# Optimization experiments

Hardware: AMD Instinct MI355X
Metric: run time of the kernel (lower is better)

Reference implementation:

```python
import jax, jax.numpy as jnp
import numpy as np

LATENT_SHAPES = [(192, 2, 2), (48, 4, 4), (24, 8, 8), (12, 16, 16), (6, 32, 32)]
B = 4          # batch
M = 32         # num_bases
HT, WT = 32, 32  # target spatial size = spatial size of z[-1] = (H/2, W/2)
EPS = 1e-3
CT = sum(s[0] for s in LATENT_SHAPES)  # 282


def _forward_fft(zs):
    # strided zero-insertion upsample of each latent to (HT, WT), concat channels, 2D FFT
    ups = []
    for zi in zs:
        b, c, h, w = zi.shape
        rh, rw = HT // h, WT // w
        u = jnp.zeros((b, c, HT, WT), zi.dtype).at[..., ::rh, ::rw].set(zi)
        ups.append(u)
    z = jnp.concatenate(ups, axis=1)            # (B, CT, HT, WT)
    return jnp.fft.fftn(z, axes=(-2, -1))       # complex64


def _inverse_fft(v_fft):
    # inverse FFT, take real part, split channels per level, strided downsample
    v = jnp.fft.ifftn(v_fft, axes=(-2, -1)).real  # (B, M, CT, HT, WT)
    splits = np.cumsum([s[0] for s in LATENT_SHAPES])[:-1]
    parts = jnp.split(v, splits, axis=-3)
    out = []
    for vi, (c, h, w) in zip(parts, LATENT_SHAPES):
        rh, rw = HT // h, WT // w
        out.append(vi[..., ::rh, ::rw])           # (B, M, c, h, w)
    return out


def _vector_field(zs, L, lam):
    z_fft = _forward_fft(zs)
    La = (L - jnp.swapaxes(L, -1, -2)).astype(jnp.complex64)        # antisymmetric (M, CT, CT)
    lam_a = (lam - jnp.roll(jnp.flip(lam, (1, 2)), (1, 1), axis=(1, 2))) * 1j  # (M, HT, WT) imaginary
    v_fft = jnp.einsum('mcd,bchw->bmdhw', La, z_fft)                 # (B, M, CT, HT, WT) complex
    v_fft = v_fft * lam_a[None, :, None, :, :]
    return _inverse_fft(v_fft)


def _log_prob(ws, zs, L, lam):
    S_ww = sum(jnp.einsum('bchw,bchw->b', wi, wi) for wi in ws)      # (B,)
    v = _vector_field(zs, L, lam)
    S_zz = sum(jnp.einsum('bnchw,bmchw->bnm', vi, vi) for vi in v)   # (B, M, M)
    S_zw = sum(jnp.einsum('bnchw,bchw->bn', vi, wi) for vi, wi in zip(v, ws))  # (B, M)
    var = jnp.maximum(jnp.mean(jnp.diagonal(S_zz, axis1=-2, axis2=-1), -1), 1e-6)
    std = jnp.sqrt(var)
    S_zz = S_zz / var[:, None, None]
    S_zw = S_zw / std[:, None]
    I = jnp.eye(M, dtype=S_zz.dtype)
    Mm = S_zz + EPS * I
    trace = EPS * S_ww + jnp.einsum('bn,bn->b', S_zw, S_zw)
    Lh = jnp.linalg.cholesky(Mm)
    logdet = 2.0 * jnp.sum(jnp.log(jnp.diagonal(Lh, axis1=-2, axis2=-1)), -1)
    return 0.5 * (logdet - trace)


def setup_inputs() -> dict:
    key = jax.random.key(0)
    ks = jax.random.split(key, 12)
    inp = {}
    for i, (c, h, w) in enumerate(LATENT_SHAPES):
        inp[f'z{i}'] = jax.random.normal(ks[i], (B, c, h, w), jnp.float32)
        inp[f'w{i}'] = jax.random.normal(ks[5 + i], (B, c, h, w), jnp.float32)
    inp['L'] = jax.random.normal(ks[10], (M, CT, CT), jnp.float32) * np.float32(1.0 / np.sqrt(CT))
    inp['lam'] = jax.random.normal(ks[11], (M, HT, WT), jnp.float32)
    return inp


def reference(z0, z1, z2, z3, z4, w0, w1, w2, w3, w4, L, lam):
    return _log_prob([w0, w1, w2, w3, w4], [z0, z1, z2, z3, z4], L, lam)
```

## Files before the change

### kernel.cpp

```cpp
#include <hip/hip_runtime.h>
#include <math.h>

#define NB 4
#define NM 32
#define CTOT 282
#define EPSV 1e-3f

__constant__ int g_cL[5]   = {192,48,24,12,6};
__constant__ int g_hL[5]   = {2,4,8,16,32};
__constant__ int g_coff[5] = {0,192,240,264,276};
__constant__ int g_zo[5]   = {0,768,1536,3072,6144};
__constant__ int g_po[4]   = {0,4,20,84};

__constant__ int t_lo[48] = {0,0,0,0,0,0,0,0,0,0,0,0,0,0,0,0,
                             0,0,0,0,0,0,0,0,0,0,0,0,0,0,0,0,
                             1,1,1,1,1,1,1,1, 2,2,2,2, 3,3, 4,4};
__constant__ int t_d0[48] = {0,6,12,18,24,30,36,42,48,54,60,66,72,78,84,90,
                             96,102,108,114,120,126,132,138,144,150,156,162,168,174,180,186,
                             192,198,204,210,216,222,228,234, 240,246,252,258, 264,270, 276,279};
__constant__ int t_nd[48] = {6,6,6,6,6,6,6,6,6,6,6,6,6,6,6,6,
                             6,6,6,6,6,6,6,6,6,6,6,6,6,6,6,6,
                             6,6,6,6,6,6,6,6, 6,6,6,6, 6,6, 3,3};

__constant__ int dft_l[30]  = {0,0,0, 1,1,1, 2,2,2,2,2,2,
                               3,3,3,3,3,3,3,3,3,3,3,3, 4,4,4,4,4,4};
__constant__ int dft_c0[30] = {0,64,128, 0,16,32, 0,4,8,12,16,20,
                               0,1,2,3,4,5,6,7,8,9,10,11, 0,1,2,3,4,5};
__constant__ int dft_nc[30] = {64,64,64, 16,16,16, 4,4,4,4,4,4,
                               1,1,1,1,1,1,1,1,1,1,1,1, 1,1,1,1,1,1};

#define N_LA     (NM*CTOT*CTOT)
#define OFF_LAT  0
#define OFF_ZRE  (OFF_LAT + N_LA)
#define OFF_ZIM  (OFF_ZRE + NB*12288)
#define OFF_WRE  (OFF_ZIM + NB*12288)
#define OFF_WIM  (OFF_WRE + NB*12288)
#define OFF_LAM  (OFF_WIM + NB*12288)
#define OFF_LAMF (OFF_LAM + NM*1024)
#define OFF_ZTR  (OFF_LAMF + NM*340)
#define OFF_ZTI  (OFF_ZTR + NB*6144)
#define OFF_UR   (OFF_ZTI + NB*6144)
#define OFF_UI   (OFF_UR + NB*NM*2720)
#define OFF_VRE  (OFF_UI + NB*NM*2720)
#define OFF_VIM  (OFF_VRE + NB*NM*12288)
#define OFF_SZZ  (OFF_VIM + NB*NM*12288)
#define OFF_SZW  (OFF_SZZ + NB*NM*NM)
#define OFF_SWW  (OFF_SZW + NB*NM)

#define PRE_LAT   (NM*25)
#define PRE_LAMF  (PRE_LAT + NM)
#define PRE_DFT   (PRE_LAMF + 2*NB*30)
#define PRE_SWW   (PRE_DFT + NB)
#define PRE_ZERO  (PRE_SWW + 17)

__global__ void __launch_bounds__(256) k_pre(
    const float* z0,const float* z1,const float* z2,const float* z3,const float* z4,
    const float* w0,const float* w1,const float* w2,const float* w3,const float* w4,
    const float* __restrict__ L, const float* __restrict__ lam, float* __restrict__ ws){
  __shared__ float shm[4160];
  int bid = blockIdx.x, t = threadIdx.x;
  if (bid < PRE_LAT){
    int m = bid/25, tl = bid%25;
    int d0 = (tl/5)*64, c0 = (tl%5)*64;
    const float* Lm = L + (size_t)m*CTOT*CTOT;
    float* At = shm;
    for (int i=t;i<4096;i+=256){
      int r=i>>6, c=i&63;
      At[r*65+c] = (c0+r<CTOT && d0+c<CTOT) ? Lm[(size_t)(c0+r)*CTOT + d0+c] : 0.f;
    }
    __syncthreads();
    float* out = ws + OFF_LAT + (size_t)m*CTOT*CTOT;
    for (int i=t;i<4096;i+=256){
      int r=i>>6, c=i&63;
      if (d0+r<CTOT && c0+c<CTOT)
        out[(size_t)(d0+r)*CTOT + c0+c] = At[c*65+r] - Lm[(size_t)(d0+r)*CTOT + c0+c];
    }
    return;
  }
  if (bid < PRE_LAMF){
    float* sA = shm;
    float* f3 = shm + 1024;
    float* f2 = shm + 1280;
    float* f1 = shm + 1344;
    int m = bid - PRE_LAT;
    for (int k=t;k<1024;k+=256){
      int ky=k>>5, kx=k&31;
      int nk = (((32-ky)&31)<<5) | ((32-kx)&31);
      float v = lam[(m<<10)+k] - lam[(m<<10)+nk];
      sA[k]=v;
      ws[OFF_LAM+(m<<10)+k]=v;
    }
    __syncthreads();
    { int s=t; int ky=s>>4, kx=s&15;
      float v = sA[(ky<<5)+kx]+sA[((ky+16)<<5)+kx]+sA[(ky<<5)+kx+16]+sA[((ky+16)<<5)+kx+16];
      f3[s]=v; ws[OFF_LAMF+m*340+84+s]=v; }
    __syncthreads();
    if (t<64){ int ky=t>>3, kx=t&7;
      float v = f3[(ky<<4)+kx]+f3[((ky+8)<<4)+kx]+f3[(ky<<4)+kx+8]+f3[((ky+8)<<4)+kx+8];
      f2[t]=v; ws[OFF_LAMF+m*340+20+t]=v; }
    __syncthreads();
    if (t<16){ int ky=t>>2, kx=t&3;
      float v = f2[(ky<<3)+kx]+f2[((ky+4)<<3)+kx]+f2[(ky<<3)+kx+4]+f2[((ky+4)<<3)+kx+4];
      f1[t]=v; ws[OFF_LAMF+m*340+4+t]=v; }
    __syncthreads();
    if (t<4){ int ky=t>>1, kx=t&1;
      float v = f1[(ky<<2)+kx]+f1[((ky+2)<<2)+kx]+f1[(ky<<2)+kx+2]+f1[((ky+2)<<2)+kx+2];
      ws[OFF_LAMF+m*340+t]=v; }
    return;
  }
  if (bid < PRE_DFT){
    float* sIn = shm;
    float* s1r = shm + 1024;
    float* s1i = shm + 2080;
    float* lc  = shm + 3136;
    float* lsn = shm + 3168;
    int i0 = bid - PRE_LAMF;
    int which = i0 / (NB*30);
    int rem = i0 % (NB*30);
    int b = rem / 30, j = rem % 30;
    int l = dft_l[j], c0 = dft_c0[j], nc = dft_nc[j];
    int h = g_hL[l], n = h*h;
    int hp = h+1, n1 = h*hp;
    int mult = 32/h;
    int elems = nc*n;
    const float* src;
    switch (which*5 + l){
      case 0: src=z0; break; case 1: src=z1; break; case 2: src=z2; break;
      case 3: src=z3; break; case 4: src=z4; break;
      case 5: src=w0; break; case 6: src=w1; break; case 7: src=w2; break;
      case 8: src=w3; break; default: src=w4; break;
    }
    for (int i=t;i<elems;i+=256) sIn[i] = src[(b*g_cL[l] + c0)*n + i];
    if (t<32){
      float ang = -6.2831853071795864f * (float)t / 32.0f;
      lc[t] = cosf(ang); lsn[t] = sinf(ang);
    }
    __syncthreads();
    for (int p=t;p<elems;p+=256){
      int p2=p%n, cc=p/n;
      int y=p2/h, kx=p2-y*h;
      float re=0.f, im=0.f;
      for (int x=0;x<h;x++){
        int id = ((kx*x)%h)*mult;
        float v = sIn[cc*n + y*h + x];
        re += v*lc[id]; im += v*lsn[id];
      }
      s1r[cc*n1 + y*hp + kx]=re; s1i[cc*n1 + y*hp + kx]=im;
    }
    __syncthreads();
    float scale = which ? 1.0f/(float)h : 1.0f;
    float* outR = ws + (which?OFF_WRE:OFF_ZRE) + b*12288 + g_zo[l] + c0*n;
    float* outI = ws + (which?OFF_WIM:OFF_ZIM) + b*12288 + g_zo[l] + c0*n;
    for (int p=t;p<elems;p+=256){
      int p2=p%n, cc=p/n;
      int ky=p2/h, kx=p2-(p2/h)*h;
      float re=0.f, im=0.f;
      for (int y=0;y<h;y++){
        int id=((ky*y)%h)*mult;
        float c=lc[id], s=lsn[id];
        float ar=s1r[cc*n1 + y*hp + kx], ai=s1i[cc*n1 + y*hp + kx];
        re += ar*c - ai*s;
        im += ar*s + ai*c;
      }
      outR[p]=re*scale; outI[p]=im*scale;
    }
    return;
  }
  if (bid < PRE_SWW){
    float* red = shm;
    int b = bid - PRE_DFT;
    const float* ptr[5] = {w0,w1,w2,w3,w4};
    float s = 0.f;
    for (int l=0;l<5;l++){
      int sz = g_cL[l]*g_hL[l]*g_hL[l];
      const float* p = ptr[l] + b*sz;
      for (int i=t;i<sz;i+=256){ float v=p[i]; s += v*v; }
    }
    red[t]=s; __syncthreads();
    for (int o=128;o>0;o>>=1){ if (t<o) red[t]+=red[t+o]; __syncthreads(); }
    if (t==0) ws[OFF_SWW + b] = red[0];
    return;
  }
  int i = (bid - PRE_SWW)*256 + t;
  if (i < NB*NM*NM + NB*NM) ws[OFF_SZZ + i] = 0.f;
}

__global__ void k_u(float* __restrict__ ws){
  __shared__ float shm[6144];
  int bid = blockIdx.x, t = threadIdx.x;
  if (bid < NB*NM*6){
    float* pr = shm;
    float* pi = shm + 1024;
    float* q3r= shm + 2048;
    float* q3i= shm + 2304;
    float* q2r= shm + 2560;
    float* q2i= shm + 2624;
    float* q1r= shm + 2688;
    float* q1i= shm + 2704;
    int c = bid%6; int m = (bid/6)%NM; int b = bid/(6*NM);
    const float* la = ws+OFF_LAM+(m<<10);
    const float* zr = ws+OFF_ZRE+b*12288+6144+(c<<10);
    const float* zi = ws+OFF_ZIM+b*12288+6144+(c<<10);
    for (int k=t;k<1024;k+=256){ float f=la[k]; pr[k]=f*zr[k]; pi[k]=f*zi[k]; }
    __syncthreads();
    size_t base = (size_t)(b*NM+m)*2720;
    float* UR = ws+OFF_UR+base; float* UI = ws+OFF_UI+base;
    { int s=t; int ky=s>>4, kx=s&15;
      float r = pr[(ky<<5)+kx]+pr[((ky+16)<<5)+kx]+pr[(ky<<5)+kx+16]+pr[((ky+16)<<5)+kx+16];
      float ii= pi[(ky<<5)+kx]+pi[((ky+16)<<5)+kx]+pi[(ky<<5)+kx+16]+pi[((ky+16)<<5)+kx+16];
      q3r[s]=r; q3i[s]=ii; UR[(84+s)*8+c]=r; UI[(84+s)*8+c]=ii; }
    __syncthreads();
    if (t<64){ int ky=t>>3, kx=t&7;
      float r = q3r[(ky<<4)+kx]+q3r[((ky+8)<<4)+kx]+q3r[(ky<<4)+kx+8]+q3r[((ky+8)<<4)+kx+8];
      float ii= q3i[(ky<<4)+kx]+q3i[((ky+8)<<4)+kx]+q3i[(ky<<4)+kx+8]+q3i[((ky+8)<<4)+kx+8];
      q2r[t]=r; q2i[t]=ii; UR[(20+t)*8+c]=r; UI[(20+t)*8+c]=ii; }
    __syncthreads();
    if (t<16){ int ky=t>>2, kx=t&3;
      float r = q2r[(ky<<3)+kx]+q2r[((ky+4)<<3)+kx]+q2r[(ky<<3)+kx+4]+q2r[((ky+4)<<3)+kx+4];
      float ii= q2i[(ky<<3)+kx]+q2i[((ky+4)<<3)+kx]+q2i[(ky<<3)+kx+4]+q2i[((ky+4)<<3)+kx+4];
      q1r[t]=r; q1i[t]=ii; UR[(4+t)*8+c]=r; UI[(4+t)*8+c]=ii; }
    __syncthreads();
    if (t<4){ int ky=t>>1, kx=t&1;
      float r = q1r[(ky<<2)+kx]+q1r[((ky+2)<<2)+kx]+q1r[(ky<<2)+kx+2]+q1r[((ky+2)<<2)+kx+2];
      float ii= q1i[(ky<<2)+kx]+q1i[((ky+2)<<2)+kx]+q1i[(ky<<2)+kx+2]+q1i[((ky+2)<<2)+kx+2];
      UR[t*8+c]=r; UI[t*8+c]=ii; }
    return;
  }
  int tid = bid - NB*NM*6;
  int b = tid>>1, ri = tid&1;
  const float* src = ws + (ri?OFF_ZIM:OFF_ZRE) + b*12288;
  float* dst = ws + (ri?OFF_ZTI:OFF_ZTR) + b*6144;
  for (int i=t;i<6144;i+=256) shm[i]=src[i];
  __syncthreads();
  for (int q=t;q<6144;q+=256){
    int s;
    if (q<768){ int bin=q/192, c=q-bin*192; s=c*4+bin; }
    else if (q<1536){ int q2=q-768; int bin=q2/48, c=q2-bin*48; s=768+c*16+bin; }
    else if (q<3072){ int q2=q-1536; int bin=q2/24, c=q2-bin*24; s=1536+c*64+bin; }
    else { int q2=q-3072; int bin=q2/12, c=q2-bin*12; s=3072+c*256+bin; }
    dst[q]=shm[s];
  }
}

__global__ void __launch_bounds__(256) k_fold(float* __restrict__ ws){
  __shared__ float smem[6160];
  float* pre   = smem;
  float* pim   = smem + 2040;
  float* sLa   = smem + 4080;
  float* c64r  = smem + 4080;
  float* c64i  = smem + 4464;
  float* c16r  = smem + 4848;
  float* c16i  = smem + 4944;
  float* c4r   = smem + 5040;
  float* c4i   = smem + 5064;
  float* lamf  = smem + 5784;
  float* ssla  = smem + 6124;

  int t = threadIdx.x, bid = blockIdx.x;
  int m    = bid / (NB*48);
  int rem  = bid % (NB*48);
  int b    = rem / 48;
  int tile = rem % 48;
  int lo = t_lo[tile], d0 = t_d0[tile], nd = t_nd[tile];
  int ho = g_hL[lo];
  int nbins = ho*ho;
  const float* zreb = ws + OFF_ZRE + b*12288;
  const float* zimb = ws + OFF_ZIM + b*12288;
  const float* ztr  = ws + OFF_ZTR + b*6144;
  const float* zti  = ws + OFF_ZTI + b*6144;
  const float* latm = ws + OFF_LAT + (size_t)m*CTOT*CTOT;

  for (int i=t;i<340;i+=256) lamf[i] = ws[OFF_LAMF + m*340 + i];
  for (int i=t;i<nd*282;i+=256){ int d=i/282, c=i-d*282; sLa[d*284+c] = latm[(size_t)(d0+d)*CTOT + c]; }
  if (t<nd*6){ int d=t/6, c=t-d*6; ssla[t] = latm[(size_t)(d0+d)*CTOT + 276 + c]; }

  int lA, kkA, c0A, offP; bool wrt;
  if (t<64){ lA=0; kkA=t&3; c0A=(t>>2)*12; offP=0; wrt=(t<4); }
  else if (t<128){ int i=t-64; lA=1; kkA=i&15; c0A=(i>>4)*12; offP=4; wrt=(i<16); }
  else { int i=t-128; lA=2; kkA=i>>1; c0A=(i&1)*12; offP=20; wrt=((i&1)==0); }
  float zAr[12], zAi[12], zBr[12], zBi[12];
  {
    int oA = g_zo[lA] + kkA*g_cL[lA] + c0A;
    const float4* zr4 = (const float4*)(ztr + oA);
    const float4* zi4 = (const float4*)(zti + oA);
    float4 x0=zr4[0], x1=zr4[1], x2=zr4[2];
    float4 y0=zi4[0], y1=zi4[1], y2=zi4[2];
    zAr[0]=x0.x;zAr[1]=x0.y;zAr[2]=x0.z;zAr[3]=x0.w;zAr[4]=x1.x;zAr[5]=x1.y;zAr[6]=x1.z;zAr[7]=x1.w;zAr[8]=x2.x;zAr[9]=x2.y;zAr[10]=x2.z;zAr[11]=x2.w;
    zAi[0]=y0.x;zAi[1]=y0.y;zAi[2]=y0.z;zAi[3]=y0.w;zAi[4]=y1.x;zAi[5]=y1.y;zAi[6]=y1.z;zAi[7]=y1.w;zAi[8]=y2.x;zAi[9]=y2.y;zAi[10]=y2.z;zAi[11]=y2.w;
    int oB = 3072 + t*12;
    const float4* zr3 = (const float4*)(ztr + oB);
    const float4* zi3 = (const float4*)(zti + oB);
    float4 p0=zr3[0], p1=zr3[1], p2=zr3[2];
    float4 q0=zi3[0], q1=zi3[1], q2=zi3[2];
    zBr[0]=p0.x;zBr[1]=p0.y;zBr[2]=p0.z;zBr[3]=p0.w;zBr[4]=p1.x;zBr[5]=p1.y;zBr[6]=p1.z;zBr[7]=p1.w;zBr[8]=p2.x;zBr[9]=p2.y;zBr[10]=p2.z;zBr[11]=p2.w;
    zBi[0]=q0.x;zBi[1]=q0.y;zBi[2]=q0.z;zBi[3]=q0.w;zBi[4]=q1.x;zBi[5]=q1.y;zBi[6]=q1.z;zBi[7]=q1.w;zBi[8]=q2.x;zBi[9]=q2.y;zBi[10]=q2.z;zBi[11]=q2.w;
  }
  __syncthreads();

  int offA = g_coff[lA] + c0A;
  for (int d=0; d<nd; d++){
    const float4* laA = (const float4*)(sLa + d*284 + offA);
    const float4* laB = (const float4*)(sLa + d*284 + 264);
    float4 a0=laA[0], a1=laA[1], a2=laA[2];
    float4 b0=laB[0], b1=laB[1], b2=laB[2];
    float av[12] = {a0.x,a0.y,a0.z,a0.w, a1.x,a1.y,a1.z,a1.w, a2.x,a2.y,a2.z,a2.w};
    float bv[12] = {b0.x,b0.y,b0.z,b0.w, b1.x,b1.y,b1.z,b1.w, b2.x,b2.y,b2.z,b2.w};
    float prA=0.f, piA=0.f, prB=0.f, piB=0.f;
    #pragma unroll
    for (int c=0;c<12;c++){ prA+=av[c]*zAr[c]; piA+=av[c]*zAi[c]; }
    #pragma unroll
    for (int c=0;c<12;c++){ prB+=bv[c]*zBr[c]; piB+=bv[c]*zBi[c]; }
    if (t<64){
      prA += __shfl_xor(prA, 4);  piA += __shfl_xor(piA, 4);
      prA += __shfl_xor(prA, 8);  piA += __shfl_xor(piA, 8);
      prA += __shfl_xor(prA,16);  piA += __shfl_xor(piA,16);
      prA += __shfl_xor(prA,32);  piA += __shfl_xor(piA,32);
    } else if (t<128){
      prA += __shfl_xor(prA,16);  piA += __shfl_xor(piA,16);
      prA += __shfl_xor(prA,32);  piA += __shfl_xor(piA,32);
    } else {
      prA += __shfl_xor(prA, 1);  piA += __shfl_xor(piA, 1);
    }
    if (wrt){ pre[d*340+offP+kkA]=prA; pim[d*340+offP+kkA]=piA; }
    pre[d*340+84+t]=prB; pim[d*340+84+t]=piB;
  }
  __syncthreads();

  float sc = (float)ho/1024.f;
  if (lo==4){
    int dlb = d0 - 276;
    const float* lamA = ws + OFF_LAM + (m<<10);
    float* vRb = ws + OFF_VRE + (size_t)(b*NM+m)*12288 + 6144 + (dlb<<10);
    float* vIb = ws + OFF_VIM + (size_t)(b*NM+m)*12288 + 6144 + (dlb<<10);
    const float* z4r = zreb + 6144;
    const float* z4i = zimb + 6144;
    for (int q=t; q<1024; q+=256){
      int ky=q>>5, kx=q&31;
      int a0=((ky&1)<<1)|(kx&1);
      int a1=4+(((ky&3)<<2)|(kx&3));
      int a2=20+(((ky&7)<<3)|(kx&7));
      int a3=84+(((ky&15)<<4)|(kx&15));
      float zr_[6], zi_[6];
      #pragma unroll
      for (int c=0;c<6;c++){ zr_[c]=z4r[(c<<10)+q]; zi_[c]=z4i[(c<<10)+q]; }
      float lm = lamA[q]*sc;
      for (int d=0; d<nd; d++){
        const float* pd = pre + d*340; const float* qd = pim + d*340;
        float Br = pd[a0]+pd[a1]+pd[a2]+pd[a3];
        float Bi = qd[a0]+qd[a1]+qd[a2]+qd[a3];
        #pragma unroll
        for (int c=0;c<6;c++){ float a=ssla[d*6+c]; Br+=a*zr_[c]; Bi+=a*zi_[c]; }
        vRb[(d<<10)+q] = -lm*Bi;
        vIb[(d<<10)+q] =  lm*Br;
      }
    }
    return;
  }

  if (lo<3){
    for (int idx=t; idx<nd*64; idx+=256){
      int d=idx>>6, k2=idx&63, ky=k2>>3, kx=k2&7;
      const float* pd = pre + d*340 + 84; const float* qd = pim + d*340 + 84;
      float r=0.f, ii=0.f;
      #pragma unroll
      for (int jy=0;jy<2;jy++)
        #pragma unroll
        for (int jx=0;jx<2;jx++){
          int a = ((ky+8*jy)<<4) | (kx+8*jx);
          float f = lamf[84+a];
          r += f*pd[a]; ii += f*qd[a];
        }
      if (lo<2){ float f=lamf[20+k2]; r+=f*pre[d*340+20+k2]; ii+=f*pim[d*340+20+k2]; }
      c64r[idx]=r; c64i[idx]=ii;
    }
  }
  __syncthreads();
  if (lo<2){
    for (int idx=t; idx<nd*16; idx+=256){
      int d=idx>>4, k2=idx&15, ky=k2>>2, kx=k2&3, base=d<<6;
      float r = c64r[base+(ky<<3)+kx]+c64r[base+((ky+4)<<3)+kx]+c64r[base+(ky<<3)+kx+4]+c64r[base+((ky+4)<<3)+kx+4];
      float ii= c64i[base+(ky<<3)+kx]+c64i[base+((ky+4)<<3)+kx]+c64i[base+(ky<<3)+kx+4]+c64i[base+((ky+4)<<3)+kx+4];
      if (lo<1){ float f=lamf[4+k2]; r+=f*pre[d*340+4+k2]; ii+=f*pim[d*340+4+k2]; }
      c16r[idx]=r; c16i[idx]=ii;
    }
  }
  __syncthreads();
  if (lo==0 && t<nd*4){
    int d=t>>2, k2=t&3, ky=k2>>1, kx=k2&1, base=d<<4;
    c4r[t]=c16r[base+(ky<<2)+kx]+c16r[base+((ky+2)<<2)+kx]+c16r[base+(ky<<2)+kx+2]+c16r[base+((ky+2)<<2)+kx+2];
    c4i[t]=c16i[base+(ky<<2)+kx]+c16i[base+((ky+2)<<2)+kx]+c16i[base+(ky<<2)+kx+2]+c16i[base+((ky+2)<<2)+kx+2];
  }
  __syncthreads();

  int dlb = d0 - g_coff[lo];
  float* vRb = ws + OFF_VRE + (size_t)(b*NM+m)*12288 + g_zo[lo];
  float* vIb = ws + OFF_VIM + (size_t)(b*NM+m)*12288 + g_zo[lo];
  const float* URg = ws + OFF_UR + (size_t)(b*NM+m)*2720;
  const float* UIg = ws + OFF_UI + (size_t)(b*NM+m)*2720;
  for (int idx=t; idx<nd*nbins; idx+=256){
    int d=idx/nbins, bin=idx-d*nbins;
    int ky=bin/ho, kx=bin-ky*ho;
    const float* pd = pre + d*340; const float* qd = pim + d*340;
    float Br = pd[((ky&1)<<1)|(kx&1)], Bi = qd[((ky&1)<<1)|(kx&1)];
    if (lo>=1){ int ix=4+(((ky&3)<<2)|(kx&3)); Br+=pd[ix]; Bi+=qd[ix]; }
    if (lo>=2){ int ix=20+(((ky&7)<<3)|(kx&7)); Br+=pd[ix]; Bi+=qd[ix]; }
    if (lo>=3){ int ix=84+(((ky&15)<<4)|(kx&15)); Br+=pd[ix]; Bi+=qd[ix]; }
    float lf = lamf[g_po[lo]+bin];
    float Vr = lf*Br, Vi = lf*Bi;
    if (lo==2){ Vr+=c64r[(d<<6)+bin]; Vi+=c64i[(d<<6)+bin]; }
    else if (lo==1){ Vr+=c16r[(d<<4)+bin]; Vi+=c16i[(d<<4)+bin]; }
    else if (lo==0){ Vr+=c4r[(d<<2)+bin]; Vi+=c4i[(d<<2)+bin]; }
    {
      int e = (g_po[lo]+bin)*8;
      const float4* ur4 = (const float4*)(URg + e);
      const float4* ui4 = (const float4*)(UIg + e);
      float4 u0=ur4[0], u1=ur4[1];
      float4 v0=ui4[0], v1=ui4[1];
      const float* sd = ssla + d*6;
      Vr += sd[0]*u0.x + sd[1]*u0.y + sd[2]*u0.z + sd[3]*u0.w + sd[4]*u1.x + sd[5]*u1.y;
      Vi += sd[0]*v0.x + sd[1]*v0.y + sd[2]*v0.z + sd[3]*v0.w + sd[4]*v1.x + sd[5]*v1.y;
    }
    int ob = (dlb+d)*nbins + bin;
    vRb[ob] = -sc*Vi;
    vIb[ob] =  sc*Vr;
  }
}

__global__ void __launch_bounds__(256) k_gram(float* __restrict__ ws){
  __shared__ float tile[32*132];
  __shared__ float wv[128];
  int t = threadIdx.x;
  int bid = blockIdx.x;
  int b = bid / 192, ch = bid % 192;
  int half = ch / 96;
  int k0 = (ch % 96) * 128;
  const float* V = ws + (half?OFF_VIM:OFF_VRE);
  const float* W = ws + (half?OFF_WIM:OFF_WRE) + b*12288 + k0;
  #pragma unroll
  for (int p=0;p<4;p++){
    int i4 = t + (p<<8);
    int row = i4 >> 5, c4 = i4 & 31;
    float4 v = *(const float4*)(V + (size_t)(b*NM+row)*12288 + k0 + (c4<<2));
    *(float4*)(tile + row*132 + (c4<<2)) = v;
  }
  if (t<128) wv[t] = W[t];
  __syncthreads();
  const float4* tf = (const float4*)tile;
  int n0 = t>>5, mm = t&31;
  float acc0=0.f, acc1=0.f, acc2=0.f, acc3=0.f;
  const float4* rm = tf + mm*33;
  const float4* r0 = tf + n0*33;
  const float4* r1 = tf + (n0+8)*33;
  const float4* r2 = tf + (n0+16)*33;
  const float4* r3 = tf + (n0+24)*33;
  for (int k4=0;k4<32;k4++){
    float4 vm = rm[k4];
    float4 v0 = r0[k4];
    float4 v1 = r1[k4];
    float4 v2 = r2[k4];
    float4 v3 = r3[k4];
    acc0 += v0.x*vm.x + v0.y*vm.y + v0.z*vm.z + v0.w*vm.w;
    acc1 += v1.x*vm.x + v1.y*vm.y + v1.z*vm.z + v1.w*vm.w;
    acc2 += v2.x*vm.x + v2.y*vm.y + v2.z*vm.z + v2.w*vm.w;
    acc3 += v3.x*vm.x + v3.y*vm.y + v3.z*vm.z + v3.w*vm.w;
  }
  float* szz = ws + OFF_SZZ + (b<<10);
  atomicAdd(&szz[(n0<<5) + mm], acc0);
  atomicAdd(&szz[((n0+8)<<5) + mm], acc1);
  atomicAdd(&szz[((n0+16)<<5) + mm], acc2);
  atomicAdd(&szz[((n0+24)<<5) + mm], acc3);
  if (t < 32){
    const float4* rn = tf + t*33;
    const float4* wf = (const float4*)wv;
    float acc=0.f;
    for (int k4=0;k4<32;k4++){
      float4 a = rn[k4]; float4 wq = wf[k4];
      acc += a.x*wq.x + a.y*wq.y + a.z*wq.z + a.w*wq.w;
    }
    atomicAdd(&ws[OFF_SZW + (b<<5) + t], acc);
  }
}

__global__ void k_final(float* __restrict__ ws, float* __restrict__ out){
  __shared__ float A[32][33];
  __shared__ float svar;
  int b = blockIdx.x, t = threadIdx.x;
  const float* szz = ws + OFF_SZZ + (b<<10);
  if (t==0){
    float s=0.f;
    for (int i=0;i<32;i++) s += szz[i*33];
    svar = fmaxf(s/32.0f, 1e-6f);
  }
  __syncthreads();
  float var = svar;
  for (int i=t;i<1024;i+=64){
    int r=i>>5, c=i&31;
    A[r][c] = szz[i]/var + ((r==c)?EPSV:0.0f);
  }
  __syncthreads();
  for (int j=0;j<32;j++){
    if (t==0) A[j][j] = sqrtf(A[j][j]);
    __syncthreads();
    if (t>j && t<32) A[t][j] /= A[j][j];
    __syncthreads();
    if (t>j && t<32){
      float lij = A[t][j];
      for (int k=j+1;k<=t;k++) A[t][k] -= lij*A[k][j];
    }
    __syncthreads();
  }
  if (t==0){
    float logdet=0.f;
    for (int j=0;j<32;j++) logdet += logf(A[j][j]);
    logdet *= 2.0f;
    const float* szw = ws + OFF_SZW + (b<<5);
    float s2=0.f;
    for (int n=0;n<32;n++) s2 += szw[n]*szw[n];
    float trace = EPSV*ws[OFF_SWW + b] + s2/var;
    out[b] = 0.5f*(logdet - trace);
  }
}

extern "C" void kernel_launch(void* const* d_in, const int* in_sizes, int n_in,
                              void* d_out, int out_size, void* d_ws, size_t ws_size,
                              hipStream_t stream){
  const float* z0 = (const float*)d_in[0];
  const float* w0 = (const float*)d_in[1];
  const float* z1 = (const float*)d_in[2];
  const float* w1 = (const float*)d_in[3];
  const float* z2 = (const float*)d_in[4];
  const float* w2 = (const float*)d_in[5];
  const float* z3 = (const float*)d_in[6];
  const float* w3 = (const float*)d_in[7];
  const float* z4 = (const float*)d_in[8];
  const float* w4 = (const float*)d_in[9];
  const float* L   = (const float*)d_in[10];
  const float* lam = (const float*)d_in[11];
  float* ws = (float*)d_ws;
  float* out = (float*)d_out;

  k_pre<<<PRE_ZERO, 256, 0, stream>>>(z0,z1,z2,z3,z4,w0,w1,w2,w3,w4, L, lam, ws);
  k_u<<<NB*NM*6 + NB*2, 256, 0, stream>>>(ws);
  k_fold<<<NB*NM*48, 256, 0, stream>>>(ws);
  k_gram<<<NB*192, 256, 0, stream>>>(ws);
  k_final<<<NB, 64, 0, stream>>>(ws, out);
}
```

Before: 201.3 us.

## Fold U-generation and z transpose into preprocessing kernel, pair antisymmetric L tiles

Removes the separate k_u launch. New blocks in k_pre recompute the level-4 DFT of z4 and lam antisymmetrisation locally, then build the multilevel U folds for 8 bases per block. The DFT blocks for z levels 0-3 now write directly in the transposed ZT layout, which drops the transpose pass. The antisymmetric L computation processes tile pairs (i,j) and (j,i) together, reading each L tile once. Each U-gen block now redoes the z4 DFT, and k_pre needs twice the shared memory.

```diff
diff --git a/kernel.cpp b/kernel.cpp
--- a/kernel.cpp
+++ b/kernel.cpp
@@ -26,8 +26,13 @@
                                3,3,3,3,3,3,3,3,3,3,3,3, 4,4,4,4,4,4};
 __constant__ int dft_c0[30] = {0,64,128, 0,16,32, 0,4,8,12,16,20,
                                0,1,2,3,4,5,6,7,8,9,10,11, 0,1,2,3,4,5};
-__constant__ int dft_nc[30] = {64,64,64, 16,16,16, 4,4,4,4,4,4,
+__constant__ int dft_nc[30] = {64,64,64, 1,16,32, 4,4,4,4,4,4,
                                1,1,1,1,1,1,1,1,1,1,1,1, 1,1,1,1,1,1};
+__constant__ int dft_nc2[30] = {64,64,64, 16,16,16, 4,4,4,4,4,4,
+                                1,1,1,1,1,1,1,1,1,1,1,1, 1,1,1,1,1,1};
+
+__constant__ int p_i[15] = {0,0,0,0,0,1,1,1,1,2,2,2,3,3,4};
+__constant__ int p_j[15] = {0,1,2,3,4,1,2,3,4,2,3,4,3,4,4};
 
 #define N_LA     (NM*CTOT*CTOT)
 #define OFF_LAT  0
@@ -47,33 +52,48 @@
 #define OFF_SZW  (OFF_SZZ + NB*NM*NM)
 #define OFF_SWW  (OFF_SZW + NB*NM)
 
-#define PRE_LAT   (NM*25)
+#define PRE_LAT   (NM*15)
 #define PRE_LAMF  (PRE_LAT + NM)
 #define PRE_DFT   (PRE_LAMF + 2*NB*30)
 #define PRE_SWW   (PRE_DFT + NB)
 #define PRE_ZERO  (PRE_SWW + 17)
+#define PRE_UGEN  (PRE_ZERO + 96)
 
 __global__ void __launch_bounds__(256) k_pre(
     const float* z0,const float* z1,const float* z2,const float* z3,const float* z4,
     const float* w0,const float* w1,const float* w2,const float* w3,const float* w4,
     const float* __restrict__ L, const float* __restrict__ lam, float* __restrict__ ws){
-  __shared__ float shm[4160];
+  __shared__ float shm[8320];
   int bid = blockIdx.x, t = threadIdx.x;
   if (bid < PRE_LAT){
-    int m = bid/25, tl = bid%25;
-    int d0 = (tl/5)*64, c0 = (tl%5)*64;
+    int m = bid/15, tl = bid%15;
+    int i64 = p_i[tl]*64, j64 = p_j[tl]*64;
     const float* Lm = L + (size_t)m*CTOT*CTOT;
-    float* At = shm;
+    float* A = shm;
+    float* B = shm + 4160;
+    bool diag = (i64==j64);
     for (int i=t;i<4096;i+=256){
       int r=i>>6, c=i&63;
-      At[r*65+c] = (c0+r<CTOT && d0+c<CTOT) ? Lm[(size_t)(c0+r)*CTOT + d0+c] : 0.f;
+      A[r*65+c] = (j64+r<CTOT && i64+c<CTOT) ? Lm[(size_t)(j64+r)*CTOT + i64+c] : 0.f;
+      if (!diag)
+        B[r*65+c] = (i64+r<CTOT && j64+c<CTOT) ? Lm[(size_t)(i64+r)*CTOT + j64+c] : 0.f;
     }
     __syncthreads();
     float* out = ws + OFF_LAT + (size_t)m*CTOT*CTOT;
-    for (int i=t;i<4096;i+=256){
-      int r=i>>6, c=i&63;
-      if (d0+r<CTOT && c0+c<CTOT)
-        out[(size_t)(d0+r)*CTOT + c0+c] = At[c*65+r] - Lm[(size_t)(d0+r)*CTOT + c0+c];
+    if (diag){
+      for (int i=t;i<4096;i+=256){
+        int r=i>>6, c=i&63;
+        if (i64+r<CTOT && j64+c<CTOT)
+          out[(size_t)(i64+r)*CTOT + j64+c] = A[c*65+r] - A[r*65+c];
+      }
+    } else {
+      for (int i=t;i<4096;i+=256){
+        int r=i>>6, c=i&63;
+        if (i64+r<CTOT && j64+c<CTOT)
+          out[(size_t)(i64+r)*CTOT + j64+c] = A[c*65+r] - B[r*65+c];
+        if (j64+r<CTOT && i64+c<CTOT)
+          out[(size_t)(j64+r)*CTOT + i64+c] = B[c*65+r] - A[r*65+c];
+      }
     }
     return;
   }
@@ -118,7 +138,7 @@
     int which = i0 / (NB*30);
     int rem = i0 % (NB*30);
     int b = rem / 30, j = rem % 30;
-    int l = dft_l[j], c0 = dft_c0[j], nc = dft_nc[j];
+    int l = dft_l[j], c0 = dft_c0[j], nc = dft_nc2[j];
     int h = g_hL[l], n = h*h;
     int hp = h+1, n1 = h*hp;
     int mult = 32/h;
@@ -149,8 +169,16 @@
     }
     __syncthreads();
     float scale = which ? 1.0f/(float)h : 1.0f;
-    float* outR = ws + (which?OFF_WRE:OFF_ZRE) + b*12288 + g_zo[l] + c0*n;
-    float* outI = ws + (which?OFF_WIM:OFF_ZIM) + b*12288 + g_zo[l] + c0*n;
+    bool zt = (which==0 && l<4);
+    float* outR;
+    float* outI;
+    if (zt){
+      outR = ws + OFF_ZTR + b*6144 + g_zo[l];
+      outI = ws + OFF_ZTI + b*6144 + g_zo[l];
+    } else {
+      outR = ws + (which?OFF_WRE:OFF_ZRE) + b*12288 + g_zo[l] + c0*n;
+      outI = ws + (which?OFF_WIM:OFF_ZIM) + b*12288 + g_zo[l] + c0*n;
+    }
     for (int p=t;p<elems;p+=256){
       int p2=p%n, cc=p/n;
       int ky=p2/h, kx=p2-(p2/h)*h;
@@ -162,7 +190,8 @@
         re += ar*c - ai*s;
         im += ar*s + ai*c;
       }
-      outR[p]=re*scale; outI[p]=im*scale;
+      int o = zt ? (p2*g_cL[l] + c0 + cc) : p;
+      outR[o]=re*scale; outI[o]=im*scale;
     }
     return;
   }
@@ -181,64 +210,96 @@
     if (t==0) ws[OFF_SWW + b] = red[0];
     return;
   }
-  int i = (bid - PRE_SWW)*256 + t;
-  if (i < NB*NM*NM + NB*NM) ws[OFF_SZZ + i] = 0.f;
-}
-
-__global__ void k_u(float* __restrict__ ws){
-  __shared__ float shm[6144];
-  int bid = blockIdx.x, t = threadIdx.x;
-  if (bid < NB*NM*6){
-    float* pr = shm;
-    float* pi = shm + 1024;
-    float* q3r= shm + 2048;
-    float* q3i= shm + 2304;
-    float* q2r= shm + 2560;
-    float* q2i= shm + 2624;
-    float* q1r= shm + 2688;
-    float* q1i= shm + 2704;
-    int c = bid%6; int m = (bid/6)%NM; int b = bid/(6*NM);
-    const float* la = ws+OFF_LAM+(m<<10);
-    const float* zr = ws+OFF_ZRE+b*12288+6144+(c<<10);
-    const float* zi = ws+OFF_ZIM+b*12288+6144+(c<<10);
-    for (int k=t;k<1024;k+=256){ float f=la[k]; pr[k]=f*zr[k]; pi[k]=f*zi[k]; }
-    __syncthreads();
-    size_t base = (size_t)(b*NM+m)*2720;
-    float* UR = ws+OFF_UR+base; float* UI = ws+OFF_UI+base;
-    { int s=t; int ky=s>>4, kx=s&15;
-      float r = pr[(ky<<5)+kx]+pr[((ky+16)<<5)+kx]+pr[(ky<<5)+kx+16]+pr[((ky+16)<<5)+kx+16];
-      float ii= pi[(ky<<5)+kx]+pi[((ky+16)<<5)+kx]+pi[(ky<<5)+kx+16]+pi[((ky+16)<<5)+kx+16];
-      q3r[s]=r; q3i[s]=ii; UR[(84+s)*8+c]=r; UI[(84+s)*8+c]=ii; }
-    __syncthreads();
-    if (t<64){ int ky=t>>3, kx=t&7;
-      float r = q3r[(ky<<4)+kx]+q3r[((ky+8)<<4)+kx]+q3r[(ky<<4)+kx+8]+q3r[((ky+8)<<4)+kx+8];
-      float ii= q3i[(ky<<4)+kx]+q3i[((ky+8)<<4)+kx]+q3i[(ky<<4)+kx+8]+q3i[((ky+8)<<4)+kx+8];
-      q2r[t]=r; q2i[t]=ii; UR[(20+t)*8+c]=r; UI[(20+t)*8+c]=ii; }
-    __syncthreads();
-    if (t<16){ int ky=t>>2, kx=t&3;
-      float r = q2r[(ky<<3)+kx]+q2r[((ky+4)<<3)+kx]+q2r[(ky<<3)+kx+4]+q2r[((ky+4)<<3)+kx+4];
-      float ii= q2i[(ky<<3)+kx]+q2i[((ky+4)<<3)+kx]+q2i[(ky<<3)+kx+4]+q2i[((ky+4)<<3)+kx+4];
-      q1r[t]=r; q1i[t]=ii; UR[(4+t)*8+c]=r; UI[(4+t)*8+c]=ii; }
-    __syncthreads();
-    if (t<4){ int ky=t>>1, kx=t&1;
-      float r = q1r[(ky<<2)+kx]+q1r[((ky+2)<<2)+kx]+q1r[(ky<<2)+kx+2]+q1r[((ky+2)<<2)+kx+2];
-      float ii= q1i[(ky<<2)+kx]+q1i[((ky+2)<<2)+kx]+q1i[(ky<<2)+kx+2]+q1i[((ky+2)<<2)+kx+2];
-      UR[t*8+c]=r; UI[t*8+c]=ii; }
+  if (bid < PRE_ZERO){
+    int i = (bid - PRE_SWW)*256 + t;
+    if (i < NB*NM*NM + NB*NM) ws[OFF_SZZ + i] = 0.f;
     return;
   }
-  int tid = bid - NB*NM*6;
-  int b = tid>>1, ri = tid&1;
-  const float* src = ws + (ri?OFF_ZIM:OFF_ZRE) + b*12288;
-  float* dst = ws + (ri?OFF_ZTI:OFF_ZTR) + b*6144;
-  for (int i=t;i<6144;i+=256) shm[i]=src[i];
-  __syncthreads();
-  for (int q=t;q<6144;q+=256){
-    int s;
-    if (q<768){ int bin=q/192, c=q-bin*192; s=c*4+bin; }
-    else if (q<1536){ int q2=q-768; int bin=q2/48, c=q2-bin*48; s=768+c*16+bin; }
-    else if (q<3072){ int q2=q-1536; int bin=q2/24, c=q2-bin*24; s=1536+c*64+bin; }
-    else { int q2=q-3072; int bin=q2/12, c=q2-bin*12; s=3072+c*256+bin; }
-    dst[q]=shm[s];
+  {
+    float* sIn = shm;
+    float* s1r = shm + 1024;
+    float* s1i = shm + 2080;
+    float* zr  = shm + 3136;
+    float* zi  = shm + 4160;
+    float* lc  = shm + 5184;
+    float* lsn = shm + 5216;
+    float* u3r = shm + 5248;
+    float* u3i = shm + 5504;
+    float* u2r = shm + 5760;
+    float* u2i = shm + 5824;
+    float* u1r = shm + 5888;
+    float* u1i = shm + 5904;
+    int idx = bid - PRE_ZERO;
+    int b = idx/24; int r2 = idx%24; int c = r2/4; int mg = r2%4;
+    const float* src = z4 + (b*6 + c)*1024;
+    for (int i=t;i<1024;i+=256) sIn[i]=src[i];
+    if (t<32){
+      float ang = -6.2831853071795864f * (float)t / 32.0f;
+      lc[t]=cosf(ang); lsn[t]=sinf(ang);
+    }
+    __syncthreads();
+    for (int p=t;p<1024;p+=256){
+      int y=p>>5, kx=p&31;
+      float re=0.f, im=0.f;
+      for (int x=0;x<32;x++){
+        int id=(kx*x)&31;
+        float v=sIn[(y<<5)+x];
+        re += v*lc[id]; im += v*lsn[id];
+      }
+      s1r[y*33+kx]=re; s1i[y*33+kx]=im;
+    }
+    __syncthreads();
+    for (int p=t;p<1024;p+=256){
+      int ky=p>>5, kx=p&31;
+      float re=0.f, im=0.f;
+      for (int y=0;y<32;y++){
+        int id=(ky*y)&31;
+        float cc=lc[id], ss=lsn[id];
+        float ar=s1r[y*33+kx], ai=s1i[y*33+kx];
+        re += ar*cc - ai*ss;
+        im += ar*ss + ai*cc;
+      }
+      zr[p]=re; zi[p]=im;
+    }
+    __syncthreads();
+    for (int mi=0; mi<8; mi++){
+      int m = mg*8 + mi;
+      const float* lm = lam + (m<<10);
+      size_t base = (size_t)(b*NM+m)*2720;
+      float* UR = ws+OFF_UR+base; float* UI = ws+OFF_UI+base;
+      {
+        int sy=t>>4, sx=t&15;
+        float ur=0.f, ui=0.f;
+        #pragma unroll
+        for (int jy=0;jy<2;jy++)
+          #pragma unroll
+          for (int jx=0;jx<2;jx++){
+            int ky=sy+16*jy, kx=sx+16*jx;
+            int k=(ky<<5)|kx;
+            int nk=(((32-ky)&31)<<5)|((32-kx)&31);
+            float la = lm[k]-lm[nk];
+            ur += la*zr[k]; ui += la*zi[k];
+          }
+        u3r[t]=ur; u3i[t]=ui;
+        UR[(84+t)*8+c]=ur; UI[(84+t)*8+c]=ui;
+      }
+      __syncthreads();
+      if (t<64){ int ky=t>>3, kx=t&7;
+        float r = u3r[(ky<<4)+kx]+u3r[((ky+8)<<4)+kx]+u3r[(ky<<4)+kx+8]+u3r[((ky+8)<<4)+kx+8];
+        float ii= u3i[(ky<<4)+kx]+u3i[((ky+8)<<4)+kx]+u3i[(ky<<4)+kx+8]+u3i[((ky+8)<<4)+kx+8];
+        u2r[t]=r; u2i[t]=ii; UR[(20+t)*8+c]=r; UI[(20+t)*8+c]=ii; }
+      __syncthreads();
+      if (t<16){ int ky=t>>2, kx=t&3;
+        float r = u2r[(ky<<3)+kx]+u2r[((ky+4)<<3)+kx]+u2r[(ky<<3)+kx+4]+u2r[((ky+4)<<3)+kx+4];
+        float ii= u2i[(ky<<3)+kx]+u2i[((ky+4)<<3)+kx]+u2i[(ky<<3)+kx+4]+u2i[((ky+4)<<3)+kx+4];
+        u1r[t]=r; u1i[t]=ii; UR[(4+t)*8+c]=r; UI[(4+t)*8+c]=ii; }
+      __syncthreads();
+      if (t<4){ int ky=t>>1, kx=t&1;
+        float r = u1r[(ky<<2)+kx]+u1r[((ky+2)<<2)+kx]+u1r[(ky<<2)+kx+2]+u1r[((ky+2)<<2)+kx+2];
+        float ii= u1i[(ky<<2)+kx]+u1i[((ky+2)<<2)+kx]+u1i[(ky<<2)+kx+2]+u1i[((ky+2)<<2)+kx+2];
+        UR[t*8+c]=r; UI[t*8+c]=ii; }
+      __syncthreads();
+    }
   }
 }
 
@@ -539,8 +600,7 @@
   float* ws = (float*)d_ws;
   float* out = (float*)d_out;
 
-  k_pre<<<PRE_ZERO, 256, 0, stream>>>(z0,z1,z2,z3,z4,w0,w1,w2,w3,w4, L, lam, ws);
-  k_u<<<NB*NM*6 + NB*2, 256, 0, stream>>>(ws);
+  k_pre<<<PRE_UGEN, 256, 0, stream>>>(z0,z1,z2,z3,z4,w0,w1,w2,w3,w4, L, lam, ws);
   k_fold<<<NB*NM*48, 256, 0, stream>>>(ws);
   k_gram<<<NB*192, 256, 0, stream>>>(ws);
   k_final<<<NB, 64, 0, stream>>>(ws, out);
```

Measured after the change: 195.9 us. -2.7%, faster.
